# Kernel tuning notes

Hardware: AMD Instinct MI355X
Metric: run time of the kernel (lower is better)

Reference implementation:

```python
import jax, jax.numpy as jnp
import numpy as np

B, F, T, D = 8, 256, 32, 1024
NEG = -1e30


def setup_inputs() -> dict:
    key = jax.random.key(0)
    ks = jax.random.split(key, 10)
    s = 1.0 / np.sqrt(D)
    return {
        "features": jax.random.normal(ks[0], (B, F, D), jnp.float32),
        "masks": jnp.ones((B, F), jnp.float32),  # unused by the module
        "textual_features": jax.random.normal(ks[1], (B, T, D), jnp.float32),
        "q_masks": jax.random.randint(ks[2], (B, T), 0, 2, jnp.int32),
        "Ws": jax.random.normal(ks[3], (D, D), jnp.float32) * s,
        "W": jax.random.normal(ks[4], (D, D), jnp.float32) * s,
        "w": jax.random.normal(ks[5], (D, 1), jnp.float32) * s,
        "b": jax.random.normal(ks[6], (1, D), jnp.float32) * s,
        "Wcw": jax.random.normal(ks[7], (1, D), jnp.float32) * s,
        "bcw": jnp.zeros((1,), jnp.float32),
        "Wcb": jax.random.normal(ks[8], (1, D), jnp.float32) * s,
        "bcb": jnp.zeros((1,), jnp.float32),
    }


def reference(features, masks, textual_features, q_masks, Ws, W, w, b, Wcw, bcw, Wcb, bcb):
    # Vectorized over all f_len frames at once (original loops over k).
    txt_proj = jnp.einsum("btd,de->bte", textual_features, Ws)   # [B,T,D]
    feat_proj = jnp.einsum("bfd,de->bfe", features, W)           # [B,F,D]
    # additive-attention hidden: [B,F,T,D]
    h = jnp.tanh(txt_proj[:, None, :, :] + feat_proj[:, :, None, :] + b[None, None, :, :][..., 0, :])
    rho = jnp.einsum("bftd,d->bft", h, w[:, 0])                  # [B,F,T]
    qm = q_masks.astype(jnp.float32)
    rho = rho + (1.0 - qm)[:, None, :] * NEG                     # mask_logits
    att = jax.nn.softmax(rho, axis=-1)                          # over t_len
    txt_h = jnp.einsum("bft,btd->bfd", att, textual_features)    # [B,F,D]
    w_s = jnp.tanh(jnp.einsum("bfd,od->bfo", txt_h, Wcw) + bcw)  # [B,F,1]
    b_s = jnp.tanh(jnp.einsum("bfd,od->bfo", txt_h, Wcb) + bcb)  # [B,F,1]
    return w_s * features + b_s
```

## Files before the change

kernel.cpp:

```cpp
#include <hip/hip_runtime.h>
#include <math.h>

#define Bdim 8
#define Fdim 256
#define Tdim 32
#define Ddim 1024
#define NEGV (-1e30f)
#define TANH_SCALE 2.8853900817779268f
#define LOG2E 1.4426950408889634f

typedef unsigned short ushort;
using short8  = __attribute__((ext_vector_type(8))) short;
using floatx4 = __attribute__((ext_vector_type(4))) float;

__device__ __forceinline__ float fexp2(float x) { return __builtin_amdgcn_exp2f(x); }
__device__ __forceinline__ float frcp(float x)  { return __builtin_amdgcn_rcpf(x); }

__device__ __forceinline__ float fast_tanh(float x) {
    return 1.0f - 2.0f * frcp(fexp2(x * TANH_SCALE) + 1.0f);
}

__device__ __forceinline__ ushort f2bf(float f) {
    unsigned u = __float_as_uint(f);
    unsigned r = u + 0x7FFFu + ((u >> 16) & 1u);
    return (ushort)(r >> 16);
}

#define GLOAD_LDS16(gp, lp) __builtin_amdgcn_global_load_lds(                   \
    (const __attribute__((address_space(1))) void*)(gp),                        \
    (__attribute__((address_space(3))) void*)(lp), 16, 0, 0)

#define WAIT_VMCNT(n) __builtin_amdgcn_s_waitcnt(((n) & 0xF) | (7 << 4) | (15 << 8) | (((n) >> 4) << 14))

__global__ __launch_bounds__(256) void prep(
    const float* __restrict__ feat, const float* __restrict__ txt,
    const float* __restrict__ W, const float* __restrict__ Ws,
    ushort* __restrict__ featB, ushort* __restrict__ txtB,
    ushort* __restrict__ WtB, ushort* __restrict__ WstB)
{
    __shared__ ushort tile[32][33];
    const int blk = blockIdx.x;
    const int NCAST = Bdim * Fdim + Bdim * Tdim;
    if (blk < NCAST) {
        const float* in; ushort* out; int base;
        if (blk < Bdim * Fdim) { in = feat; out = featB; base = blk * Ddim; }
        else { in = txt; out = txtB; base = (blk - Bdim * Fdim) * Ddim; }
        const int i = base + threadIdx.x * 4;
        float4 v = *(const float4*)(in + i);
        ushort4 o;
        o.x = f2bf(v.x); o.y = f2bf(v.y); o.z = f2bf(v.z); o.w = f2bf(v.w);
        *(ushort4*)(out + i) = o;
    } else {
        int t = blk - NCAST;
        const float* in = (t < 1024) ? W : Ws;
        ushort* out = (t < 1024) ? WtB : WstB;
        t &= 1023;
        const int bx = (t & 31) * 32;
        const int by = (t >> 5) * 32;
        const int tx = threadIdx.x & 31;
        const int tg = threadIdx.x >> 5;
        #pragma unroll
        for (int r = tg; r < 32; r += 8)
            tile[r][tx] = f2bf(in[(size_t)(by + r) * Ddim + bx + tx]);
        __syncthreads();
        #pragma unroll
        for (int r = tg; r < 32; r += 8)
            out[(size_t)(bx + r) * Ddim + by + tx] = tile[tx][r];
    }
}

#define GBM 128
#define GBN 64
#define GBK 32

__global__ __launch_bounds__(512, 4) void gemm_dual(
    const ushort* __restrict__ A1, const ushort* __restrict__ Bt1, float* __restrict__ C1,
    const ushort* __restrict__ A2, const ushort* __restrict__ Bt2, float* __restrict__ C2,
    const float* __restrict__ bias2)
{
    const int K = Ddim, N = Ddim;
    const int by = blockIdx.y;
    const ushort* A; const ushort* Bt; float* C; const float* bias; int m0;
    if (by < 16) { A = A1; Bt = Bt1; C = C1; bias = nullptr; m0 = by * GBM; }
    else         { A = A2; Bt = Bt2; C = C2; bias = bias2;  m0 = (by - 16) * GBM; }
    const int n0 = blockIdx.x * GBN;

    __shared__ __align__(16) ushort As[2][GBM * GBK];
    __shared__ __align__(16) ushort Bs[2][GBN * GBK];

    const int tid  = threadIdx.x;
    const int l    = tid & 63;
    const int wave = tid >> 6;

    const int wm = (wave >> 1) * 32;
    const int wn = (wave & 1) * 32;

    floatx4 acc[2][2];
    #pragma unroll
    for (int i = 0; i < 2; ++i)
        #pragma unroll
        for (int j = 0; j < 2; ++j)
            acc[i][j] = (floatx4){0.0f, 0.0f, 0.0f, 0.0f};

    const int lm = l & 15;
    const int lk = (l >> 4) * 8;

    const int crow = l >> 2;
    const int ccol = (l & 3) * 8;

    const ushort* aSrc = A  + (size_t)(m0 + wave * 16 + crow) * K + ccol;
    const ushort* bSrc = Bt + (size_t)(n0 + wave * 16 + crow) * K + ccol;
    const int aOff = (wave * 16) * GBK;
    const int bOff = (wave * 16) * GBK;
    const bool doB = (wave < 4);

    const int NK = K / GBK;

    GLOAD_LDS16(aSrc, &As[0][aOff]);
    if (doB) GLOAD_LDS16(bSrc, &Bs[0][bOff]);

    for (int i = 0; i < NK; ++i) {
        const int cur = i & 1;
        if (i + 1 < NK) {
            const int kn = (i + 1) * GBK;
            const int nxt = cur ^ 1;
            GLOAD_LDS16(aSrc + kn, &As[nxt][aOff]);
            if (doB) {
                GLOAD_LDS16(bSrc + kn, &Bs[nxt][bOff]);
                WAIT_VMCNT(2);
            } else {
                WAIT_VMCNT(1);
            }
        } else {
            WAIT_VMCNT(0);
        }
        __builtin_amdgcn_s_barrier();

        short8 af0 = *(const short8*)&As[cur][(wm +  0 + lm) * GBK + lk];
        short8 af1 = *(const short8*)&As[cur][(wm + 16 + lm) * GBK + lk];
        short8 bf0 = *(const short8*)&Bs[cur][(wn +  0 + lm) * GBK + lk];
        short8 bf1 = *(const short8*)&Bs[cur][(wn + 16 + lm) * GBK + lk];
        acc[0][0] = __builtin_amdgcn_mfma_f32_16x16x32_bf16(af0, bf0, acc[0][0], 0, 0, 0);
        acc[0][1] = __builtin_amdgcn_mfma_f32_16x16x32_bf16(af0, bf1, acc[0][1], 0, 0, 0);
        acc[1][0] = __builtin_amdgcn_mfma_f32_16x16x32_bf16(af1, bf0, acc[1][0], 0, 0, 0);
        acc[1][1] = __builtin_amdgcn_mfma_f32_16x16x32_bf16(af1, bf1, acc[1][1], 0, 0, 0);

        __builtin_amdgcn_s_barrier();
    }

    const int rowq = (l >> 4) * 4;
    #pragma unroll
    for (int im = 0; im < 2; ++im) {
        #pragma unroll
        for (int in_ = 0; in_ < 2; ++in_) {
            const int col = n0 + wn + in_ * 16 + lm;
            float badd = (bias != nullptr) ? bias[col] : 0.0f;
            #pragma unroll
            for (int r = 0; r < 4; ++r) {
                const int row = m0 + wm + im * 16 + rowq + r;
                C[(size_t)row * N + col] = fexp2((acc[im][in_][r] + badd) * TANH_SCALE);
            }
        }
    }
}

__global__ __launch_bounds__(256, 4) void attn_fused(
    const float* __restrict__ feat,
    const float* __restrict__ txt,
    const int*   __restrict__ qmask,
    const float* __restrict__ fp_s,
    const float* __restrict__ tp_s,
    const float* __restrict__ wvec,
    const float* __restrict__ Wcw,
    const float* __restrict__ bcw,
    const float* __restrict__ Wcb,
    const float* __restrict__ bcb,
    float* __restrict__ out)
{
    const int blk  = blockIdx.x;
    const int f0   = blk * 2;
    const int b    = f0 >> 8;
    const int tid  = threadIdx.x;
    const int lane = tid & 63;
    const int wave = tid >> 6;

    __shared__ float part[2][Tdim][68];
    __shared__ float srho[2][Tdim];
    __shared__ float satt[2][Tdim];
    __shared__ float sred[4][4];

    float4 wv[4], fva[4], fvb[4];
    const float* fr0 = fp_s + (size_t)f0 * Ddim;
    const float* fr1 = fr0 + Ddim;
    #pragma unroll
    for (int it = 0; it < 4; ++it) {
        const int d = lane * 4 + it * 256;
        wv[it]  = *(const float4*)&wvec[d];
        fva[it] = *(const float4*)&fr0[d];
        fvb[it] = *(const float4*)&fr1[d];
    }
    float sumw = 0.0f;
    #pragma unroll
    for (int it = 0; it < 4; ++it)
        sumw += wv[it].x + wv[it].y + wv[it].z + wv[it].w;
    #pragma unroll
    for (int off = 32; off; off >>= 1) sumw += __shfl_xor(sumw, off, 64);

    const float* tpb = tp_s + (size_t)b * Tdim * Ddim;
    float s0[8], s1[8];
    float4 cur[4], nxt[4];
    {
        const float* tr = tpb + (size_t)(wave * 8) * Ddim;
        #pragma unroll
        for (int it = 0; it < 4; ++it)
            cur[it] = *(const float4*)&tr[lane * 4 + it * 256];
    }
    #pragma unroll
    for (int tt = 0; tt < 8; ++tt) {
        if (tt < 7) {
            const float* trn = tpb + (size_t)(wave * 8 + tt + 1) * Ddim;
            #pragma unroll
            for (int it = 0; it < 4; ++it)
                nxt[it] = *(const float4*)&trn[lane * 4 + it * 256];
        }
        float a0 = 0.0f, b0 = 0.0f, a1 = 0.0f, b1 = 0.0f;
        #pragma unroll
        for (int it = 0; it < 4; ++it) {
            float4 tv = cur[it];
            float e, r;
            e = tv.x * fva[it].x; r = frcp(e + 1.0f); a0 = fmaf(wv[it].x, r, a0);
            e = tv.y * fva[it].y; r = frcp(e + 1.0f); b0 = fmaf(wv[it].y, r, b0);
            e = tv.z * fva[it].z; r = frcp(e + 1.0f); a0 = fmaf(wv[it].z, r, a0);
            e = tv.w * fva[it].w; r = frcp(e + 1.0f); b0 = fmaf(wv[it].w, r, b0);
            e = tv.x * fvb[it].x; r = frcp(e + 1.0f); a1 = fmaf(wv[it].x, r, a1);
            e = tv.y * fvb[it].y; r = frcp(e + 1.0f); b1 = fmaf(wv[it].y, r, b1);
            e = tv.z * fvb[it].z; r = frcp(e + 1.0f); a1 = fmaf(wv[it].z, r, a1);
            e = tv.w * fvb[it].w; r = frcp(e + 1.0f); b1 = fmaf(wv[it].w, r, b1);
        }
        s0[tt] = a0 + b0;
        s1[tt] = a1 + b1;
        #pragma unroll
        for (int it = 0; it < 4; ++it) cur[it] = nxt[it];
    }
    #pragma unroll
    for (int tt = 0; tt < 8; ++tt) {
        part[0][wave * 8 + tt][lane] = s0[tt];
        part[1][wave * 8 + tt][lane] = s1[tt];
    }
    __syncthreads();

    {
        const int pair = tid >> 2, q = tid & 3;
        const int f = pair >> 5, t = pair & 31;
        const float* src = &part[f][t][q * 16];
        float4 v0 = *(const float4*)(src);
        float4 v1 = *(const float4*)(src + 4);
        float4 v2 = *(const float4*)(src + 8);
        float4 v3 = *(const float4*)(src + 12);
        float sum = ((v0.x + v0.y) + (v0.z + v0.w))
                  + ((v1.x + v1.y) + (v1.z + v1.w))
                  + ((v2.x + v2.y) + (v2.z + v2.w))
                  + ((v3.x + v3.y) + (v3.z + v3.w));
        sum += __shfl_xor(sum, 1, 64);
        sum += __shfl_xor(sum, 2, 64);
        if (q == 0) srho[f][t] = sum;
    }
    __syncthreads();

    if (wave == 0) {
        const int f = lane >> 5, t = lane & 31;
        const float q = (float)qmask[b * Tdim + t];
        float L = sumw - 2.0f * srho[f][t] + (1.0f - q) * NEGV;
        float m = L;
        #pragma unroll
        for (int off = 16; off; off >>= 1) m = fmaxf(m, __shfl_xor(m, off, 64));
        float e = fexp2((L - m) * LOG2E);
        float ssum = e;
        #pragma unroll
        for (int off = 16; off; off >>= 1) ssum += __shfl_xor(ssum, off, 64);
        satt[f][t] = e * frcp(ssum);
    }
    __syncthreads();

    const float* txtb = txt + (size_t)b * Tdim * Ddim;
    const int d0 = tid * 4;
    float4 th0 = {0,0,0,0}, th1 = {0,0,0,0};
    #pragma unroll 8
    for (int t = 0; t < Tdim; ++t) {
        float4 tv = *(const float4*)&txtb[(size_t)t * Ddim + d0];
        const float a0 = satt[0][t], a1 = satt[1][t];
        th0.x = fmaf(a0, tv.x, th0.x); th0.y = fmaf(a0, tv.y, th0.y);
        th0.z = fmaf(a0, tv.z, th0.z); th0.w = fmaf(a0, tv.w, th0.w);
        th1.x = fmaf(a1, tv.x, th1.x); th1.y = fmaf(a1, tv.y, th1.y);
        th1.z = fmaf(a1, tv.z, th1.z); th1.w = fmaf(a1, tv.w, th1.w);
    }

    float4 wcw = *(const float4*)&Wcw[d0];
    float4 wcb = *(const float4*)&Wcb[d0];
    float p00 = th0.x*wcw.x + th0.y*wcw.y + th0.z*wcw.z + th0.w*wcw.w;
    float p01 = th0.x*wcb.x + th0.y*wcb.y + th0.z*wcb.z + th0.w*wcb.w;
    float p10 = th1.x*wcw.x + th1.y*wcw.y + th1.z*wcw.z + th1.w*wcw.w;
    float p11 = th1.x*wcb.x + th1.y*wcb.y + th1.z*wcb.z + th1.w*wcb.w;
    #pragma unroll
    for (int off = 32; off; off >>= 1) {
        p00 += __shfl_xor(p00, off, 64);
        p01 += __shfl_xor(p01, off, 64);
        p10 += __shfl_xor(p10, off, 64);
        p11 += __shfl_xor(p11, off, 64);
    }
    if (lane == 0) {
        sred[wave][0] = p00; sred[wave][1] = p01;
        sred[wave][2] = p10; sred[wave][3] = p11;
    }
    __syncthreads();
    const float c00 = sred[0][0] + sred[1][0] + sred[2][0] + sred[3][0];
    const float c01 = sred[0][1] + sred[1][1] + sred[2][1] + sred[3][1];
    const float c10 = sred[0][2] + sred[1][2] + sred[2][2] + sred[3][2];
    const float c11 = sred[0][3] + sred[1][3] + sred[2][3] + sred[3][3];
    const float ws0 = fast_tanh(c00 + bcw[0]);
    const float bs0 = fast_tanh(c01 + bcb[0]);
    const float ws1 = fast_tanh(c10 + bcw[0]);
    const float bs1 = fast_tanh(c11 + bcb[0]);

    const float* ft0 = feat + (size_t)f0 * Ddim;
    float4 v0 = *(const float4*)&ft0[d0];
    float4 v1 = *(const float4*)&ft0[Ddim + d0];
    float4 o0, o1;
    o0.x = fmaf(ws0, v0.x, bs0); o0.y = fmaf(ws0, v0.y, bs0);
    o0.z = fmaf(ws0, v0.z, bs0); o0.w = fmaf(ws0, v0.w, bs0);
    o1.x = fmaf(ws1, v1.x, bs1); o1.y = fmaf(ws1, v1.y, bs1);
    o1.z = fmaf(ws1, v1.z, bs1); o1.w = fmaf(ws1, v1.w, bs1);
    *(float4*)&out[(size_t)f0 * Ddim + d0] = o0;
    *(float4*)&out[(size_t)f0 * Ddim + Ddim + d0] = o1;
}

extern "C" void kernel_launch(void* const* d_in, const int* in_sizes, int n_in,
                              void* d_out, int out_size, void* d_ws, size_t ws_size,
                              hipStream_t stream) {
    const float* features = (const float*)d_in[0];
    const float* textual  = (const float*)d_in[2];
    const int*   q_masks  = (const int*)d_in[3];
    const float* Ws       = (const float*)d_in[4];
    const float* W        = (const float*)d_in[5];
    const float* wvec     = (const float*)d_in[6];
    const float* bvec     = (const float*)d_in[7];
    const float* Wcw      = (const float*)d_in[8];
    const float* bcw      = (const float*)d_in[9];
    const float* Wcb      = (const float*)d_in[10];
    const float* bcb      = (const float*)d_in[11];
    float* out = (float*)d_out;

    float*  fp_ws = (float*)d_ws;
    float*  tp_ws = fp_ws + (size_t)Bdim * Fdim * Ddim;
    ushort* featB = (ushort*)(tp_ws + (size_t)Bdim * Tdim * Ddim);
    ushort* txtB  = featB + (size_t)Bdim * Fdim * Ddim;
    ushort* WtB   = txtB + (size_t)Bdim * Tdim * Ddim;
    ushort* WstB  = WtB + (size_t)Ddim * Ddim;

    prep<<<Bdim * Fdim + Bdim * Tdim + 2048, 256, 0, stream>>>(
        features, textual, W, Ws, featB, txtB, WtB, WstB);
    gemm_dual<<<dim3(Ddim / GBN, 18), 512, 0, stream>>>(
        featB, WtB, fp_ws, txtB, WstB, tp_ws, bvec);
    attn_fused<<<(Bdim * Fdim) / 2, 256, 0, stream>>>(
        features, textual, q_masks, fp_ws, tp_ws,
        wvec, Wcw, bcw, Wcb, bcb, out);
}
```

Baseline: 122.2 us.

## Pair reciprocals in the attention score loop and widen the GEMM N tile

```diff
diff --git a/kernel.cpp b/kernel.cpp
--- a/kernel.cpp
+++ b/kernel.cpp
@@ -70,7 +70,7 @@
 }
 
 #define GBM 128
-#define GBN 64
+#define GBN 128
 #define GBK 32
 
 __global__ __launch_bounds__(512, 4) void gemm_dual(
@@ -93,13 +93,13 @@
     const int wave = tid >> 6;
 
     const int wm = (wave >> 1) * 32;
-    const int wn = (wave & 1) * 32;
-
-    floatx4 acc[2][2];
+    const int wn = (wave & 1) * 64;
+
+    floatx4 acc[2][4];
     #pragma unroll
     for (int i = 0; i < 2; ++i)
         #pragma unroll
-        for (int j = 0; j < 2; ++j)
+        for (int j = 0; j < 4; ++j)
             acc[i][j] = (floatx4){0.0f, 0.0f, 0.0f, 0.0f};
 
     const int lm = l & 15;
@@ -112,12 +112,11 @@
     const ushort* bSrc = Bt + (size_t)(n0 + wave * 16 + crow) * K + ccol;
     const int aOff = (wave * 16) * GBK;
     const int bOff = (wave * 16) * GBK;
-    const bool doB = (wave < 4);
 
     const int NK = K / GBK;
 
     GLOAD_LDS16(aSrc, &As[0][aOff]);
-    if (doB) GLOAD_LDS16(bSrc, &Bs[0][bOff]);
+    GLOAD_LDS16(bSrc, &Bs[0][bOff]);
 
     for (int i = 0; i < NK; ++i) {
         const int cur = i & 1;
@@ -125,12 +124,8 @@
             const int kn = (i + 1) * GBK;
             const int nxt = cur ^ 1;
             GLOAD_LDS16(aSrc + kn, &As[nxt][aOff]);
-            if (doB) {
-                GLOAD_LDS16(bSrc + kn, &Bs[nxt][bOff]);
-                WAIT_VMCNT(2);
-            } else {
-                WAIT_VMCNT(1);
-            }
+            GLOAD_LDS16(bSrc + kn, &Bs[nxt][bOff]);
+            WAIT_VMCNT(2);
         } else {
             WAIT_VMCNT(0);
         }
@@ -140,10 +135,16 @@
         short8 af1 = *(const short8*)&As[cur][(wm + 16 + lm) * GBK + lk];
         short8 bf0 = *(const short8*)&Bs[cur][(wn +  0 + lm) * GBK + lk];
         short8 bf1 = *(const short8*)&Bs[cur][(wn + 16 + lm) * GBK + lk];
+        short8 bf2 = *(const short8*)&Bs[cur][(wn + 32 + lm) * GBK + lk];
+        short8 bf3 = *(const short8*)&Bs[cur][(wn + 48 + lm) * GBK + lk];
         acc[0][0] = __builtin_amdgcn_mfma_f32_16x16x32_bf16(af0, bf0, acc[0][0], 0, 0, 0);
         acc[0][1] = __builtin_amdgcn_mfma_f32_16x16x32_bf16(af0, bf1, acc[0][1], 0, 0, 0);
+        acc[0][2] = __builtin_amdgcn_mfma_f32_16x16x32_bf16(af0, bf2, acc[0][2], 0, 0, 0);
+        acc[0][3] = __builtin_amdgcn_mfma_f32_16x16x32_bf16(af0, bf3, acc[0][3], 0, 0, 0);
         acc[1][0] = __builtin_amdgcn_mfma_f32_16x16x32_bf16(af1, bf0, acc[1][0], 0, 0, 0);
         acc[1][1] = __builtin_amdgcn_mfma_f32_16x16x32_bf16(af1, bf1, acc[1][1], 0, 0, 0);
+        acc[1][2] = __builtin_amdgcn_mfma_f32_16x16x32_bf16(af1, bf2, acc[1][2], 0, 0, 0);
+        acc[1][3] = __builtin_amdgcn_mfma_f32_16x16x32_bf16(af1, bf3, acc[1][3], 0, 0, 0);
 
         __builtin_amdgcn_s_barrier();
     }
@@ -152,7 +153,7 @@
     #pragma unroll
     for (int im = 0; im < 2; ++im) {
         #pragma unroll
-        for (int in_ = 0; in_ < 2; ++in_) {
+        for (int in_ = 0; in_ < 4; ++in_) {
             const int col = n0 + wn + in_ * 16 + lm;
             float badd = (bias != nullptr) ? bias[col] : 0.0f;
             #pragma unroll
@@ -226,16 +227,25 @@
         float a0 = 0.0f, b0 = 0.0f, a1 = 0.0f, b1 = 0.0f;
         #pragma unroll
         for (int it = 0; it < 4; ++it) {
-            float4 tv = cur[it];
-            float e, r;
-            e = tv.x * fva[it].x; r = frcp(e + 1.0f); a0 = fmaf(wv[it].x, r, a0);
-            e = tv.y * fva[it].y; r = frcp(e + 1.0f); b0 = fmaf(wv[it].y, r, b0);
-            e = tv.z * fva[it].z; r = frcp(e + 1.0f); a0 = fmaf(wv[it].z, r, a0);
-            e = tv.w * fva[it].w; r = frcp(e + 1.0f); b0 = fmaf(wv[it].w, r, b0);
-            e = tv.x * fvb[it].x; r = frcp(e + 1.0f); a1 = fmaf(wv[it].x, r, a1);
-            e = tv.y * fvb[it].y; r = frcp(e + 1.0f); b1 = fmaf(wv[it].y, r, b1);
-            e = tv.z * fvb[it].z; r = frcp(e + 1.0f); a1 = fmaf(wv[it].z, r, a1);
-            e = tv.w * fvb[it].w; r = frcp(e + 1.0f); b1 = fmaf(wv[it].w, r, b1);
+            const float4 tv  = cur[it];
+            const float4 wvi = wv[it];
+            float q1, q2, num;
+            q1 = fmaf(tv.x, fva[it].x, 1.0f);
+            q2 = fmaf(tv.y, fva[it].y, 1.0f);
+            num = fmaf(wvi.x, q2, wvi.y * q1);
+            a0 = fmaf(num, frcp(q1 * q2), a0);
+            q1 = fmaf(tv.z, fva[it].z, 1.0f);
+            q2 = fmaf(tv.w, fva[it].w, 1.0f);
+            num = fmaf(wvi.z, q2, wvi.w * q1);
+            b0 = fmaf(num, frcp(q1 * q2), b0);
+            q1 = fmaf(tv.x, fvb[it].x, 1.0f);
+            q2 = fmaf(tv.y, fvb[it].y, 1.0f);
+            num = fmaf(wvi.x, q2, wvi.y * q1);
+            a1 = fmaf(num, frcp(q1 * q2), a1);
+            q1 = fmaf(tv.z, fvb[it].z, 1.0f);
+            q2 = fmaf(tv.w, fvb[it].w, 1.0f);
+            num = fmaf(wvi.z, q2, wvi.w * q1);
+            b1 = fmaf(num, frcp(q1 * q2), b1);
         }
         s0[tt] = a0 + b0;
         s1[tt] = a1 + b1;
```

After: 121.2 us, median of 2. No clear change (-0.9%).
